# Kernel tuning notes

Measured on AMD Instinct MI355X. Metric: run time of the kernel, lower is better.

Reference implementation:

```python
import jax, jax.numpy as jnp
import numpy as np

B, S, D = 2, 2048, 1024
H_Q, H_KV, DK, DV = 16, 8, 64, 64
R = H_Q // H_KV  # q heads per kv head (GQA)
THETA = 10000.0


def setup_inputs() -> dict:
    key = jax.random.key(0)
    ks = jax.random.split(key, 12)
    inv_freq = 1.0 / (THETA ** (jnp.arange(0, DK, 2, dtype=jnp.float32) / DK))  # [DK/2]
    angles = jnp.arange(S, dtype=jnp.float32)[:, None] * inv_freq[None, :]      # [S, DK/2]
    scale = 0.02
    return {
        "x": jax.random.normal(ks[0], (B, S, D), jnp.float32),
        "Wq": jax.random.normal(ks[1], (D, H_Q * DK), jnp.float32) * scale,
        "bq": jnp.zeros((H_Q * DK,), jnp.float32),
        "Wk": jax.random.normal(ks[2], (D, H_KV * DK), jnp.float32) * scale,
        "bk": jnp.zeros((H_KV * DK,), jnp.float32),
        "Wv": jax.random.normal(ks[3], (D, H_KV * DV), jnp.float32) * scale,
        "bv": jnp.zeros((H_KV * DV,), jnp.float32),
        "Wo": jax.random.normal(ks[4], (H_Q * DV, D), jnp.float32) * scale,
        "bo": jnp.zeros((D,), jnp.float32),
        "freqs_cos": jnp.cos(angles),
        "freqs_sin": jnp.sin(angles),
        "attention_mask": jax.random.bernoulli(ks[5], 0.9, (B, S)),  # True = real token
    }


def _rope(t, cos, sin):
    # t: [B, S, H, Dh]; cos/sin: [S, Dh/2]. Complex rotation on interleaved pairs.
    tp = t.reshape(*t.shape[:-1], -1, 2)
    x1, x2 = tp[..., 0], tp[..., 1]
    c = cos[None, :, None, :]
    s = sin[None, :, None, :]
    o1 = x1 * c - x2 * s
    o2 = x1 * s + x2 * c
    return jnp.stack([o1, o2], axis=-1).reshape(t.shape)


def reference(x, Wq, bq, Wk, bk, Wv, bv, Wo, bo, freqs_cos, freqs_sin, attention_mask):
    b, s, _ = x.shape
    q = (x @ Wq + bq).reshape(b, s, H_Q, DK)
    k = (x @ Wk + bk).reshape(b, s, H_KV, DK)
    v = (x @ Wv + bv).reshape(b, s, H_KV, DV)
    q = _rope(q, freqs_cos, freqs_sin)
    k = _rope(k, freqs_cos, freqs_sin)
    q = q.transpose(0, 2, 1, 3)                      # [B, Hq, S, DK]
    k = jnp.repeat(k.transpose(0, 2, 1, 3), R, axis=1)  # GQA expand -> [B, Hq, S, DK]
    v = jnp.repeat(v.transpose(0, 2, 1, 3), R, axis=1)  # [B, Hq, S, DV]
    causal = jnp.tril(jnp.ones((s, s), dtype=bool))
    # Module does logical_or(padding, causal) -- replicated faithfully.
    mask = jnp.logical_or(attention_mask[:, None, None, :], causal[None, None])
    scale = 1.0 / jnp.sqrt(jnp.float32(DK))
    scores = jnp.einsum('bhqd,bhkd->bhqk', q, k) * scale
    scores = jnp.where(mask, scores, -jnp.inf)
    attn = jax.nn.softmax(scores, axis=-1)
    out = jnp.einsum('bhqk,bhkd->bhqd', attn, v)
    out = out.transpose(0, 2, 1, 3).reshape(b, s, H_Q * DV)
    return out @ Wo + bo
```

## Files before the change

kernel.cpp:

```cpp
#include <hip/hip_runtime.h>
#include <hip/hip_bf16.h>
#include <math.h>

typedef __attribute__((ext_vector_type(8))) short bf16x8;
typedef __attribute__((ext_vector_type(4))) float f32x4;

#define OFF_XB  0ull
#define OFF_WT  (8ull<<20)
#define OFF_WO  (12ull<<20)
#define OFF_QB  (14ull<<20)
#define OFF_KB  (22ull<<20)
#define OFF_VT  (26ull<<20)
#define OFF_AO  (30ull<<20)
#define OFF_MB  (38ull<<20)

#define QSCALE 0.18033688056680276f

__device__ inline unsigned pack_bf162(float a, float b) {
    __hip_bfloat162 t = __float22bfloat162_rn(make_float2(a, b));
    return *(unsigned*)&t;
}

__device__ inline float exp2_fast(float x) {
    float r;
    asm("v_exp_f32 %0, %1" : "=v"(r) : "v"(x));
    return r;
}

__device__ inline void gload16(const void* g, void* l) {
    __builtin_amdgcn_global_load_lds(
        (const __attribute__((address_space(1))) void*)g,
        (__attribute__((address_space(3))) void*)l, 16, 0, 0);
}

__launch_bounds__(256)
__global__ void prep_kernel(const float* __restrict__ x,
                            const float* __restrict__ Wq, const float* __restrict__ Wk,
                            const float* __restrict__ Wv, const float* __restrict__ Wo,
                            const void* __restrict__ mraw,
                            __hip_bfloat16* __restrict__ XB,
                            __hip_bfloat16* __restrict__ WT,
                            __hip_bfloat16* __restrict__ WoT,
                            float* __restrict__ mbias) {
    __shared__ float T[32][33];
    __shared__ int bad01, badf;
    const int tid = threadIdx.x;
    const int bid = blockIdx.x;
    if (bid < 1024) {
        const int base = bid * 4096;
#pragma unroll
        for (int i = 0; i < 4; ++i) {
            const int e = base + (i * 256 + tid) * 4;
            const float4 v = *(const float4*)&x[e];
            uint2 pk;
            pk.x = pack_bf162(v.x, v.y);
            pk.y = pack_bf162(v.z, v.w);
            *(uint2*)&XB[e] = pk;
        }
    } else if (bid < 4096) {
        const float* src; int ldn, nbase; __hip_bfloat16* dst; int n0, k0;
        if (bid < 3072) {
            const int tb = bid - 1024;
            const int kt = tb >> 6, nt = tb & 63;
            n0 = nt * 32; k0 = kt * 32; dst = WT;
            if (n0 < 1024)      { src = Wq; ldn = 1024; nbase = n0; }
            else if (n0 < 1536) { src = Wk; ldn = 512;  nbase = n0 - 1024; }
            else                { src = Wv; ldn = 512;  nbase = n0 - 1536; }
        } else {
            const int tb = bid - 3072;
            const int kt = tb >> 5, nt = tb & 31;
            n0 = nt * 32; k0 = kt * 32; dst = WoT;
            src = Wo; ldn = 1024; nbase = n0;
        }
        const int c = tid & 31, r0 = tid >> 5;
#pragma unroll
        for (int i = 0; i < 4; ++i)
            T[r0 + 8 * i][c] = src[(size_t)(k0 + r0 + 8 * i) * ldn + nbase + c];
        __syncthreads();
#pragma unroll
        for (int i = 0; i < 4; ++i) {
            const int nn = r0 + 8 * i;
            dst[(size_t)(n0 + nn) * 1024 + k0 + c] = __float2bfloat16(T[c][nn]);
        }
    } else {
        if (tid == 0) { bad01 = 0; badf = 0; }
        __syncthreads();
        const unsigned* w = (const unsigned*)mraw;
#pragma unroll
        for (int i = 0; i < 4; ++i) {
            const unsigned v = w[tid * 4 + i];
            if (v > 1u) atomicAdd(&bad01, 1);
            if (v != 0u && v != 0x3F800000u) atomicAdd(&badf, 1);
        }
        __syncthreads();
        const int fmt = (bad01 == 0) ? 0 : ((badf == 0) ? 1 : 2);
        for (int i = tid; i < 4096; i += 256) {
            bool on;
            if (fmt == 2) on = (((const unsigned char*)mraw)[i] != 0);
            else          on = (w[i] != 0u);
            mbias[i] = on ? 0.f : -1e30f;
        }
    }
}

#define QSTAGE(SEL, K0_) do {                                                    \
    _Pragma("unroll") for (int rnd_ = 0; rnd_ < 4; ++rnd_) {                     \
        const int off_ = rnd_ * 4096 + wid * 1024 + lane * 16;                   \
        const int row_ = off_ >> 7;                                              \
        const int ch_  = ((off_ >> 4) & 7) ^ (row_ & 7);                         \
        gload16((const char*)Ag + ((size_t)(n0 + row_) * 1024 + (K0_) + ch_ * 8) * 2, \
                Asm + (SEL) * 16384 + rnd_ * 4096 + wid * 1024);                 \
        gload16((const char*)Bg + ((size_t)(m0 + row_) * 1024 + (K0_) + ch_ * 8) * 2, \
                Bsm + (SEL) * 16384 + rnd_ * 4096 + wid * 1024);                 \
    }                                                                            \
} while (0)

__launch_bounds__(256)
__global__ void qkv_mfma_kernel(const __hip_bfloat16* __restrict__ XB,
                                const __hip_bfloat16* __restrict__ WT,
                                const float* __restrict__ bq, const float* __restrict__ bk,
                                const float* __restrict__ bv,
                                const float* __restrict__ fc, const float* __restrict__ fs,
                                __hip_bfloat16* __restrict__ QB,
                                __hip_bfloat16* __restrict__ KB,
                                __hip_bfloat16* __restrict__ VT) {
    __shared__ __attribute__((aligned(16))) char Asm[32768];
    __shared__ __attribute__((aligned(16))) char Bsm[32768];
    const int tid = threadIdx.x;
    const int lane = tid & 63, wid = tid >> 6;
    const int c = lane & 15, g = lane >> 4;
    const int n0 = blockIdx.x * 128, m0 = blockIdx.y * 128;
    const int wn = (wid >> 1) * 64, wm = (wid & 1) * 64;
    const __hip_bfloat16* Ag = WT;
    const __hip_bfloat16* Bg = XB;

    f32x4 acc[4][4];
#pragma unroll
    for (int ni = 0; ni < 4; ++ni)
#pragma unroll
        for (int mj = 0; mj < 4; ++mj) acc[ni][mj] = f32x4{0.f, 0.f, 0.f, 0.f};

    QSTAGE(0, 0);
    int cur = 0;
    for (int kt = 0; kt < 16; ++kt) {
        const int k0 = kt * 64;
        if (kt < 15) {
            QSTAGE(cur ^ 1, k0 + 64);
            asm volatile("s_waitcnt vmcnt(8)" ::: "memory");
        } else {
            asm volatile("s_waitcnt vmcnt(0)" ::: "memory");
        }
        __builtin_amdgcn_sched_barrier(0);
        __builtin_amdgcn_s_barrier();
        __builtin_amdgcn_sched_barrier(0);

        const char* Ac = Asm + cur * 16384;
        const char* Bc = Bsm + cur * 16384;
#pragma unroll
        for (int ks = 0; ks < 2; ++ks) {
            bf16x8 af[4], bfr[4];
#pragma unroll
            for (int t = 0; t < 4; ++t) {
                const int sl = ((g + 4 * ks) ^ (c & 7)) << 4;
                af[t]  = *(const bf16x8*)(Ac + (wn + 16 * t + c) * 128 + sl);
                bfr[t] = *(const bf16x8*)(Bc + (wm + 16 * t + c) * 128 + sl);
            }
#pragma unroll
            for (int ni = 0; ni < 4; ++ni)
#pragma unroll
                for (int mj = 0; mj < 4; ++mj)
                    acc[ni][mj] = __builtin_amdgcn_mfma_f32_16x16x32_bf16(
                        af[ni], bfr[mj], acc[ni][mj], 0, 0, 0);
        }
        __builtin_amdgcn_sched_barrier(0);
        __builtin_amdgcn_s_barrier();
        __builtin_amdgcn_sched_barrier(0);
        cur ^= 1;
    }

#pragma unroll
    for (int ni = 0; ni < 4; ++ni) {
        const int nb = n0 + wn + 16 * ni + 4 * g;
        const float* bias; int nloc;
        if (nb < 1024)      { bias = bq; nloc = nb; }
        else if (nb < 1536) { bias = bk; nloc = nb - 1024; }
        else                { bias = bv; nloc = nb - 1536; }
        const float4 b4 = *(const float4*)&bias[nloc];
        const int h = nloc >> 6, dk = nb & 63;
#pragma unroll
        for (int mj = 0; mj < 4; ++mj) {
            const int tok = m0 + wm + 16 * mj + c;
            const int bb = tok >> 11, sp = tok & 2047;
            float v0 = acc[ni][mj][0] + b4.x;
            float v1 = acc[ni][mj][1] + b4.y;
            float v2 = acc[ni][mj][2] + b4.z;
            float v3 = acc[ni][mj][3] + b4.w;
            if (nb < 1536) {
                const int p = sp * 32 + (dk >> 1);
                const float c0 = fc[p], s0 = fs[p];
                const float c1 = fc[p + 1], s1 = fs[p + 1];
                float o0 = v0 * c0 - v1 * s0, o1 = v0 * s0 + v1 * c0;
                float o2 = v2 * c1 - v3 * s1, o3 = v2 * s1 + v3 * c1;
                uint2 pk;
                if (nb < 1024) {
                    o0 *= QSCALE; o1 *= QSCALE; o2 *= QSCALE; o3 *= QSCALE;
                    pk.x = pack_bf162(o0, o1); pk.y = pack_bf162(o2, o3);
                    *(uint2*)&QB[(size_t)((bb * 16 + h) * 2048 + sp) * 64 + dk] = pk;
                } else {
                    pk.x = pack_bf162(o0, o1); pk.y = pack_bf162(o2, o3);
                    *(uint2*)&KB[(size_t)((bb * 8 + h) * 2048 + sp) * 64 + dk] = pk;
                }
            } else {
                const size_t vb = (size_t)((bb * 8 + h) * 64 + dk) * 2048 + sp;
                VT[vb]          = __float2bfloat16(v0);
                VT[vb + 2048]   = __float2bfloat16(v1);
                VT[vb + 4096]   = __float2bfloat16(v2);
                VT[vb + 6144]   = __float2bfloat16(v3);
            }
        }
    }
}

__launch_bounds__(256)
__global__ void out_mfma_kernel(const __hip_bfloat16* __restrict__ AOB,
                                const __hip_bfloat16* __restrict__ WoT,
                                const float* __restrict__ bo,
                                float* __restrict__ out) {
    __shared__ __attribute__((aligned(16))) char Asm[32768];
    __shared__ __attribute__((aligned(16))) char Bsm[32768];
    const int tid = threadIdx.x;
    const int lane = tid & 63, wid = tid >> 6;
    const int c = lane & 15, g = lane >> 4;
    const int n0 = blockIdx.x * 128, m0 = blockIdx.y * 128;
    const int wn = (wid >> 1) * 64, wm = (wid & 1) * 64;
    const __hip_bfloat16* Ag = WoT;
    const __hip_bfloat16* Bg = AOB;

    f32x4 acc[4][4];
#pragma unroll
    for (int ni = 0; ni < 4; ++ni)
#pragma unroll
        for (int mj = 0; mj < 4; ++mj) acc[ni][mj] = f32x4{0.f, 0.f, 0.f, 0.f};

    QSTAGE(0, 0);
    int cur = 0;
    for (int kt = 0; kt < 16; ++kt) {
        const int k0 = kt * 64;
        if (kt < 15) {
            QSTAGE(cur ^ 1, k0 + 64);
            asm volatile("s_waitcnt vmcnt(8)" ::: "memory");
        } else {
            asm volatile("s_waitcnt vmcnt(0)" ::: "memory");
        }
        __builtin_amdgcn_sched_barrier(0);
        __builtin_amdgcn_s_barrier();
        __builtin_amdgcn_sched_barrier(0);

        const char* Ac = Asm + cur * 16384;
        const char* Bc = Bsm + cur * 16384;
#pragma unroll
        for (int ks = 0; ks < 2; ++ks) {
            bf16x8 af[4], bfr[4];
#pragma unroll
            for (int t = 0; t < 4; ++t) {
                const int sl = ((g + 4 * ks) ^ (c & 7)) << 4;
                af[t]  = *(const bf16x8*)(Ac + (wn + 16 * t + c) * 128 + sl);
                bfr[t] = *(const bf16x8*)(Bc + (wm + 16 * t + c) * 128 + sl);
            }
#pragma unroll
            for (int ni = 0; ni < 4; ++ni)
#pragma unroll
                for (int mj = 0; mj < 4; ++mj)
                    acc[ni][mj] = __builtin_amdgcn_mfma_f32_16x16x32_bf16(
                        af[ni], bfr[mj], acc[ni][mj], 0, 0, 0);
        }
        __builtin_amdgcn_sched_barrier(0);
        __builtin_amdgcn_s_barrier();
        __builtin_amdgcn_sched_barrier(0);
        cur ^= 1;
    }
#pragma unroll
    for (int ni = 0; ni < 4; ++ni) {
        const int nb = n0 + wn + 16 * ni + 4 * g;
        const float4 b4 = *(const float4*)&bo[nb];
#pragma unroll
        for (int mj = 0; mj < 4; ++mj) {
            const int tok = m0 + wm + 16 * mj + c;
            const f32x4 a = acc[ni][mj];
            const float4 st = make_float4(a[0] + b4.x, a[1] + b4.y,
                                          a[2] + b4.z, a[3] + b4.w);
            *(float4*)&out[(size_t)tok * 1024 + nb] = st;
        }
    }
}


#define STAGE(BUFSEL, K0_) do {                                                  \
    _Pragma("unroll") for (int rnd_ = 0; rnd_ < 2; ++rnd_) {                     \
        const int off_ = rnd_ * 4096 + tid * 16;                                 \
        const int row_ = off_ >> 7;                                              \
        const int ch_  = ((off_ >> 4) & 7) ^ (row_ & 7);                         \
        gload16(Kh + (size_t)((K0_) + row_) * 64 + ch_ * 8,                      \
                Ksm + (BUFSEL) * 8192 + rnd_ * 4096 + wid * 1024);               \
        gload16(Vh + (size_t)row_ * 2048 + (K0_) + ch_ * 8,                      \
                Vsm + (BUFSEL) * 8192 + rnd_ * 4096 + wid * 1024);               \
    }                                                                            \
} while (0)

__launch_bounds__(256)
__global__ void attn_kernel(const __hip_bfloat16* __restrict__ QB,
                            const __hip_bfloat16* __restrict__ KB,
                            const __hip_bfloat16* __restrict__ VT,
                            const float* __restrict__ maskb,
                            __hip_bfloat16* __restrict__ AOB) {
    __shared__ __attribute__((aligned(16))) char Ksm[16384];
    __shared__ __attribute__((aligned(16))) char Vsm[16384];
    __shared__ char P_lds[4][4096];

    const int tid  = threadIdx.x;
    const int lane = tid & 63, wid = tid >> 6;
    const int c = lane & 15, g = lane >> 4;

    const int bid = blockIdx.x;
    const int o_  = (bid & 7) * 64 + (bid >> 3);
    const int qx = o_ & 15, h = (o_ >> 4) & 15, b = o_ >> 8;
    const int qb = qx * 128 + wid * 32;

    const __hip_bfloat16* Qh = QB + (size_t)(b * 16 + h)       * 2048 * 64;
    const __hip_bfloat16* Kh = KB + (size_t)(b * 8 + (h >> 1)) * 2048 * 64;
    const __hip_bfloat16* Vh = VT + (size_t)(b * 8 + (h >> 1)) * 64 * 2048;
    const float* mb = maskb + b * 2048;

    STAGE(0, 0);

    bf16x8 bq[2][2];
#pragma unroll
    for (int rt = 0; rt < 2; ++rt)
#pragma unroll
        for (int ks = 0; ks < 2; ++ks)
            bq[rt][ks] = *(const bf16x8*)&Qh[(size_t)(qb + 16 * rt + c) * 64
                                             + 32 * ks + 8 * g];
    __syncthreads();

    const short oneb = (short)0x3F80;
    const bf16x8 ones = {oneb, oneb, oneb, oneb, oneb, oneb, oneb, oneb};

    f32x4 o[2][4];
    f32x4 lacc[2];
#pragma unroll
    for (int rt = 0; rt < 2; ++rt) {
        lacc[rt] = f32x4{0.f, 0.f, 0.f, 0.f};
#pragma unroll
        for (int mt = 0; mt < 4; ++mt) o[rt][mt] = f32x4{0.f, 0.f, 0.f, 0.f};
    }
    float m_[2] = {-INFINITY, -INFINITY};

    char* Pw = &P_lds[wid][0];
    const int swz = (c & 7) << 4;

    int cur = 0;
    for (int kt = 0; kt < 32; ++kt) {
        const int k0 = kt * 64;
        if (kt < 31) {
            STAGE(cur ^ 1, k0 + 64);
            asm volatile("s_waitcnt vmcnt(4)" ::: "memory");
        } else {
            asm volatile("s_waitcnt vmcnt(0)" ::: "memory");
        }
        __builtin_amdgcn_sched_barrier(0);
        __builtin_amdgcn_s_barrier();
        __builtin_amdgcn_sched_barrier(0);

        const char* Kc = Ksm + cur * 8192;
        const char* Vc = Vsm + cur * 8192;

        bf16x8 ak[4][2];
#pragma unroll
        for (int mt = 0; mt < 4; ++mt)
#pragma unroll
            for (int ks = 0; ks < 2; ++ks)
                ak[mt][ks] = *(const bf16x8*)(Kc + (16 * mt + c) * 128
                                              + (((g + 4 * ks) ^ (c & 7)) << 4));

        const bool needb = (k0 + 63 > qb);
        f32x4 bv4[4];
        if (needb) {
#pragma unroll
            for (int mt = 0; mt < 4; ++mt)
                bv4[mt] = *(const f32x4*)&mb[k0 + 16 * mt + 4 * g];
        }

        __builtin_amdgcn_s_setprio(1);
        f32x4 st[2][4];
#pragma unroll
        for (int rt = 0; rt < 2; ++rt)
#pragma unroll
            for (int mt = 0; mt < 4; ++mt) {
                f32x4 z = f32x4{0.f, 0.f, 0.f, 0.f};
                z = __builtin_amdgcn_mfma_f32_16x16x32_bf16(ak[mt][0], bq[rt][0], z, 0, 0, 0);
                z = __builtin_amdgcn_mfma_f32_16x16x32_bf16(ak[mt][1], bq[rt][1], z, 0, 0, 0);
                st[rt][mt] = z;
            }
        __builtin_amdgcn_s_setprio(0);

        bf16x8 av[4][2];
#pragma unroll
        for (int mt = 0; mt < 4; ++mt)
#pragma unroll
            for (int ks = 0; ks < 2; ++ks)
                av[mt][ks] = *(const bf16x8*)(Vc + (16 * mt + c) * 128
                                              + (((g + 4 * ks) ^ (c & 7)) << 4));

#pragma unroll
        for (int rt = 0; rt < 2; ++rt) {
            const int qw = qb + 16 * rt;
            if (k0 + 63 <= qw) {
            } else if (k0 > qw + 15) {
#pragma unroll
                for (int mt = 0; mt < 4; ++mt)
                    st[rt][mt] = st[rt][mt] + bv4[mt];
            } else {
                const int qg = qw + c;
#pragma unroll
                for (int mt = 0; mt < 4; ++mt)
#pragma unroll
                    for (int r = 0; r < 4; ++r) {
                        const int kg = k0 + 16 * mt + 4 * g + r;
                        st[rt][mt][r] += (kg <= qg) ? 0.f : bv4[mt][r];
                    }
            }
            const f32x4 m01 = __builtin_elementwise_max(st[rt][0], st[rt][1]);
            const f32x4 m23 = __builtin_elementwise_max(st[rt][2], st[rt][3]);
            const f32x4 mv  = __builtin_elementwise_max(m01, m23);
            float pmax = fmaxf(fmaxf(mv[0], mv[1]), fmaxf(mv[2], mv[3]));
            pmax = fmaxf(pmax, __shfl_xor(pmax, 16));
            pmax = fmaxf(pmax, __shfl_xor(pmax, 32));
            if (!__all(pmax <= m_[rt] + 11.5f)) {
                const float mn = fmaxf(m_[rt], pmax);
                const float alpha = exp2_fast(m_[rt] - mn);
                m_[rt] = mn;
                lacc[rt][0] *= alpha;
#pragma unroll
                for (int mt = 0; mt < 4; ++mt) o[rt][mt] *= alpha;
            }
            const float mneg = m_[rt];
            const f32x4 m4 = {mneg, mneg, mneg, mneg};
#pragma unroll
            for (int mt = 0; mt < 4; ++mt) {
                const f32x4 e = st[rt][mt] - m4;
#pragma unroll
                for (int r = 0; r < 4; ++r)
                    st[rt][mt][r] = exp2_fast(e[r]);
            }

            char* Pr = Pw + rt * 2048 + c * 128;
#pragma unroll
            for (int mt = 0; mt < 4; ++mt) {
                const unsigned w0 = pack_bf162(st[rt][mt][0], st[rt][mt][1]);
                const unsigned w1 = pack_bf162(st[rt][mt][2], st[rt][mt][3]);
                *(unsigned long long*)(Pr + ((32 * mt + 8 * g) ^ swz)) =
                    (unsigned long long)w0 | ((unsigned long long)w1 << 32);
            }
        }

#pragma unroll
        for (int rt = 0; rt < 2; ++rt) {
            const char* Pr = Pw + rt * 2048 + c * 128;
            const bf16x8 pb0 = *(const bf16x8*)(Pr + ((16 * g) ^ swz));
            const bf16x8 pb1 = *(const bf16x8*)(Pr + ((64 + 16 * g) ^ swz));
            __builtin_amdgcn_s_setprio(1);
#pragma unroll
            for (int mt = 0; mt < 4; ++mt) {
                o[rt][mt] = __builtin_amdgcn_mfma_f32_16x16x32_bf16(av[mt][0], pb0, o[rt][mt], 0, 0, 0);
                o[rt][mt] = __builtin_amdgcn_mfma_f32_16x16x32_bf16(av[mt][1], pb1, o[rt][mt], 0, 0, 0);
            }
            lacc[rt] = __builtin_amdgcn_mfma_f32_16x16x32_bf16(ones, pb0, lacc[rt], 0, 0, 0);
            lacc[rt] = __builtin_amdgcn_mfma_f32_16x16x32_bf16(ones, pb1, lacc[rt], 0, 0, 0);
            __builtin_amdgcn_s_setprio(0);
        }

        __builtin_amdgcn_sched_barrier(0);
        __builtin_amdgcn_s_barrier();
        __builtin_amdgcn_sched_barrier(0);
        cur ^= 1;
    }

#pragma unroll
    for (int rt = 0; rt < 2; ++rt) {
        const float inv = 1.f / lacc[rt][0];
        const size_t tok = (size_t)(b * 2048 + qb + 16 * rt + c);
#pragma unroll
        for (int mt = 0; mt < 4; ++mt) {
            uint2 pk;
            pk.x = pack_bf162(o[rt][mt][0] * inv, o[rt][mt][1] * inv);
            pk.y = pack_bf162(o[rt][mt][2] * inv, o[rt][mt][3] * inv);
            *(uint2*)&AOB[tok * 1024 + h * 64 + 16 * mt + 4 * g] = pk;
        }
    }
}

extern "C" void kernel_launch(void* const* d_in, const int* in_sizes, int n_in,
                              void* d_out, int out_size, void* d_ws, size_t ws_size,
                              hipStream_t stream) {
    const float* x  = (const float*)d_in[0];
    const float* Wq = (const float*)d_in[1];
    const float* bq = (const float*)d_in[2];
    const float* Wk = (const float*)d_in[3];
    const float* bk = (const float*)d_in[4];
    const float* Wv = (const float*)d_in[5];
    const float* bv = (const float*)d_in[6];
    const float* Wo = (const float*)d_in[7];
    const float* bo = (const float*)d_in[8];
    const float* fc = (const float*)d_in[9];
    const float* fs = (const float*)d_in[10];
    const void*  am = d_in[11];

    char* ws = (char*)d_ws;
    __hip_bfloat16* XB  = (__hip_bfloat16*)(ws + OFF_XB);
    __hip_bfloat16* WT  = (__hip_bfloat16*)(ws + OFF_WT);
    __hip_bfloat16* WoT = (__hip_bfloat16*)(ws + OFF_WO);
    __hip_bfloat16* QB  = (__hip_bfloat16*)(ws + OFF_QB);
    __hip_bfloat16* KB  = (__hip_bfloat16*)(ws + OFF_KB);
    __hip_bfloat16* VT  = (__hip_bfloat16*)(ws + OFF_VT);
    __hip_bfloat16* AOB = (__hip_bfloat16*)(ws + OFF_AO);
    float* mbias = (float*)(ws + OFF_MB);
    float* out   = (float*)d_out;

    hipLaunchKernelGGL(prep_kernel, dim3(4097), dim3(256), 0, stream,
                       x, Wq, Wk, Wv, Wo, am, XB, WT, WoT, mbias);
    hipLaunchKernelGGL(qkv_mfma_kernel, dim3(16, 32), dim3(256), 0, stream,
                       XB, WT, bq, bk, bv, fc, fs, QB, KB, VT);
    hipLaunchKernelGGL(attn_kernel, dim3(512), dim3(256), 0, stream,
                       QB, KB, VT, mbias, AOB);
    hipLaunchKernelGGL(out_mfma_kernel, dim3(8, 32), dim3(256), 0, stream,
                       AOB, WoT, bo, out);
}
```

Before: 141.3 us.

## Widen attention KV tile to 128 keys with per-row-tile PV fusion

The attention loop now processes 128 keys per iteration instead of 64, halving the number of barriers and loop iterations. The double-buffered K/V tiles in LDS double to 32 KB each, and V uses a 16-way swizzle for its 256-byte rows. The P write and PV MFMAs are fused per row tile, V fragments are reloaded from LDS per k-slice, and launch bounds ask for 2 blocks per CU. This raises register pressure and LDS use (about 80 KB per block), which may limit occupancy.

After: 132.0 us (median of 2 runs). 6.6% less time.

```diff
diff --git a/kernel.cpp b/kernel.cpp
--- a/kernel.cpp
+++ b/kernel.cpp
@@ -295,26 +295,28 @@
 }
 
 
-#define STAGE(BUFSEL, K0_) do {                                                  \
-    _Pragma("unroll") for (int rnd_ = 0; rnd_ < 2; ++rnd_) {                     \
-        const int off_ = rnd_ * 4096 + tid * 16;                                 \
-        const int row_ = off_ >> 7;                                              \
-        const int ch_  = ((off_ >> 4) & 7) ^ (row_ & 7);                         \
-        gload16(Kh + (size_t)((K0_) + row_) * 64 + ch_ * 8,                      \
-                Ksm + (BUFSEL) * 8192 + rnd_ * 4096 + wid * 1024);               \
-        gload16(Vh + (size_t)row_ * 2048 + (K0_) + ch_ * 8,                      \
-                Vsm + (BUFSEL) * 8192 + rnd_ * 4096 + wid * 1024);               \
+#define STAGE128(SEL, K0_) do {                                                  \
+    _Pragma("unroll") for (int rnd_ = 0; rnd_ < 4; ++rnd_) {                     \
+        const int off_ = rnd_ * 4096 + wid * 1024 + lane * 16;                   \
+        const int kr_ = off_ >> 7;                                               \
+        const int kc_ = ((off_ >> 4) & 7) ^ (kr_ & 7);                           \
+        gload16(Kh + (size_t)((K0_) + kr_) * 64 + kc_ * 8,                       \
+                Ksm + (SEL) * 16384 + rnd_ * 4096 + wid * 1024);                 \
+        const int vr_ = off_ >> 8;                                               \
+        const int vc_ = ((off_ >> 4) & 15) ^ (vr_ & 15);                         \
+        gload16(Vh + (size_t)vr_ * 2048 + (K0_) + vc_ * 8,                       \
+                Vsm + (SEL) * 16384 + rnd_ * 4096 + wid * 1024);                 \
     }                                                                            \
 } while (0)
 
-__launch_bounds__(256)
+__launch_bounds__(256, 2)
 __global__ void attn_kernel(const __hip_bfloat16* __restrict__ QB,
                             const __hip_bfloat16* __restrict__ KB,
                             const __hip_bfloat16* __restrict__ VT,
                             const float* __restrict__ maskb,
                             __hip_bfloat16* __restrict__ AOB) {
-    __shared__ __attribute__((aligned(16))) char Ksm[16384];
-    __shared__ __attribute__((aligned(16))) char Vsm[16384];
+    __shared__ __attribute__((aligned(16))) char Ksm[32768];
+    __shared__ __attribute__((aligned(16))) char Vsm[32768];
     __shared__ char P_lds[4][4096];
 
     const int tid  = threadIdx.x;
@@ -331,7 +333,7 @@
     const __hip_bfloat16* Vh = VT + (size_t)(b * 8 + (h >> 1)) * 64 * 2048;
     const float* mb = maskb + b * 2048;
 
-    STAGE(0, 0);
+    STAGE128(0, 0);
 
     bf16x8 bq[2][2];
 #pragma unroll
@@ -355,15 +357,15 @@
     }
     float m_[2] = {-INFINITY, -INFINITY};
 
-    char* Pw = &P_lds[wid][0];
+    char* Pr = &P_lds[wid][0] + c * 256;
     const int swz = (c & 7) << 4;
 
     int cur = 0;
-    for (int kt = 0; kt < 32; ++kt) {
-        const int k0 = kt * 64;
-        if (kt < 31) {
-            STAGE(cur ^ 1, k0 + 64);
-            asm volatile("s_waitcnt vmcnt(4)" ::: "memory");
+    for (int kt = 0; kt < 16; ++kt) {
+        const int k0 = kt * 128;
+        if (kt < 15) {
+            STAGE128(cur ^ 1, k0 + 128);
+            asm volatile("s_waitcnt vmcnt(8)" ::: "memory");
         } else {
             asm volatile("s_waitcnt vmcnt(0)" ::: "memory");
         }
@@ -371,67 +373,65 @@
         __builtin_amdgcn_s_barrier();
         __builtin_amdgcn_sched_barrier(0);
 
-        const char* Kc = Ksm + cur * 8192;
-        const char* Vc = Vsm + cur * 8192;
-
-        bf16x8 ak[4][2];
-#pragma unroll
-        for (int mt = 0; mt < 4; ++mt)
-#pragma unroll
-            for (int ks = 0; ks < 2; ++ks)
-                ak[mt][ks] = *(const bf16x8*)(Kc + (16 * mt + c) * 128
-                                              + (((g + 4 * ks) ^ (c & 7)) << 4));
-
-        const bool needb = (k0 + 63 > qb);
-        f32x4 bv4[4];
+        const char* Kc = Ksm + cur * 16384;
+        const char* Vc = Vsm + cur * 16384;
+
+        const bool needb = (k0 + 127 > qb);
+        f32x4 bv4[8];
         if (needb) {
 #pragma unroll
+            for (int mt = 0; mt < 8; ++mt)
+                bv4[mt] = *(const f32x4*)&mb[k0 + 16 * mt + 4 * g];
+        }
+
+        f32x4 st[2][8];
+        __builtin_amdgcn_s_setprio(1);
+#pragma unroll
+        for (int hf = 0; hf < 2; ++hf) {
+            bf16x8 ak[4][2];
+#pragma unroll
             for (int mt = 0; mt < 4; ++mt)
-                bv4[mt] = *(const f32x4*)&mb[k0 + 16 * mt + 4 * g];
-        }
-
-        __builtin_amdgcn_s_setprio(1);
-        f32x4 st[2][4];
-#pragma unroll
-        for (int rt = 0; rt < 2; ++rt)
-#pragma unroll
-            for (int mt = 0; mt < 4; ++mt) {
-                f32x4 z = f32x4{0.f, 0.f, 0.f, 0.f};
-                z = __builtin_amdgcn_mfma_f32_16x16x32_bf16(ak[mt][0], bq[rt][0], z, 0, 0, 0);
-                z = __builtin_amdgcn_mfma_f32_16x16x32_bf16(ak[mt][1], bq[rt][1], z, 0, 0, 0);
-                st[rt][mt] = z;
-            }
+#pragma unroll
+                for (int ks = 0; ks < 2; ++ks)
+                    ak[mt][ks] = *(const bf16x8*)(Kc + (64 * hf + 16 * mt + c) * 128
+                                                  + (((g + 4 * ks) ^ (c & 7)) << 4));
+#pragma unroll
+            for (int rt = 0; rt < 2; ++rt)
+#pragma unroll
+                for (int mt = 0; mt < 4; ++mt) {
+                    f32x4 z = f32x4{0.f, 0.f, 0.f, 0.f};
+                    z = __builtin_amdgcn_mfma_f32_16x16x32_bf16(ak[mt][0], bq[rt][0], z, 0, 0, 0);
+                    z = __builtin_amdgcn_mfma_f32_16x16x32_bf16(ak[mt][1], bq[rt][1], z, 0, 0, 0);
+                    st[rt][4 * hf + mt] = z;
+                }
+        }
         __builtin_amdgcn_s_setprio(0);
-
-        bf16x8 av[4][2];
-#pragma unroll
-        for (int mt = 0; mt < 4; ++mt)
-#pragma unroll
-            for (int ks = 0; ks < 2; ++ks)
-                av[mt][ks] = *(const bf16x8*)(Vc + (16 * mt + c) * 128
-                                              + (((g + 4 * ks) ^ (c & 7)) << 4));
 
 #pragma unroll
         for (int rt = 0; rt < 2; ++rt) {
             const int qw = qb + 16 * rt;
-            if (k0 + 63 <= qw) {
+            if (k0 + 127 <= qw) {
             } else if (k0 > qw + 15) {
 #pragma unroll
-                for (int mt = 0; mt < 4; ++mt)
+                for (int mt = 0; mt < 8; ++mt)
                     st[rt][mt] = st[rt][mt] + bv4[mt];
             } else {
                 const int qg = qw + c;
 #pragma unroll
-                for (int mt = 0; mt < 4; ++mt)
+                for (int mt = 0; mt < 8; ++mt)
 #pragma unroll
                     for (int r = 0; r < 4; ++r) {
                         const int kg = k0 + 16 * mt + 4 * g + r;
                         st[rt][mt][r] += (kg <= qg) ? 0.f : bv4[mt][r];
                     }
             }
-            const f32x4 m01 = __builtin_elementwise_max(st[rt][0], st[rt][1]);
-            const f32x4 m23 = __builtin_elementwise_max(st[rt][2], st[rt][3]);
-            const f32x4 mv  = __builtin_elementwise_max(m01, m23);
+            const f32x4 a0 = __builtin_elementwise_max(st[rt][0], st[rt][1]);
+            const f32x4 a1 = __builtin_elementwise_max(st[rt][2], st[rt][3]);
+            const f32x4 a2 = __builtin_elementwise_max(st[rt][4], st[rt][5]);
+            const f32x4 a3 = __builtin_elementwise_max(st[rt][6], st[rt][7]);
+            const f32x4 b0 = __builtin_elementwise_max(a0, a1);
+            const f32x4 b1 = __builtin_elementwise_max(a2, a3);
+            const f32x4 mv = __builtin_elementwise_max(b0, b1);
             float pmax = fmaxf(fmaxf(mv[0], mv[1]), fmaxf(mv[2], mv[3]));
             pmax = fmaxf(pmax, __shfl_xor(pmax, 16));
             pmax = fmaxf(pmax, __shfl_xor(pmax, 32));
@@ -446,36 +446,35 @@
             const float mneg = m_[rt];
             const f32x4 m4 = {mneg, mneg, mneg, mneg};
 #pragma unroll
-            for (int mt = 0; mt < 4; ++mt) {
+            for (int mt = 0; mt < 8; ++mt) {
                 const f32x4 e = st[rt][mt] - m4;
 #pragma unroll
                 for (int r = 0; r < 4; ++r)
                     st[rt][mt][r] = exp2_fast(e[r]);
             }
 
-            char* Pr = Pw + rt * 2048 + c * 128;
-#pragma unroll
-            for (int mt = 0; mt < 4; ++mt) {
+#pragma unroll
+            for (int mt = 0; mt < 8; ++mt) {
                 const unsigned w0 = pack_bf162(st[rt][mt][0], st[rt][mt][1]);
                 const unsigned w1 = pack_bf162(st[rt][mt][2], st[rt][mt][3]);
                 *(unsigned long long*)(Pr + ((32 * mt + 8 * g) ^ swz)) =
                     (unsigned long long)w0 | ((unsigned long long)w1 << 32);
             }
-        }
-
-#pragma unroll
-        for (int rt = 0; rt < 2; ++rt) {
-            const char* Pr = Pw + rt * 2048 + c * 128;
-            const bf16x8 pb0 = *(const bf16x8*)(Pr + ((16 * g) ^ swz));
-            const bf16x8 pb1 = *(const bf16x8*)(Pr + ((64 + 16 * g) ^ swz));
+
             __builtin_amdgcn_s_setprio(1);
 #pragma unroll
-            for (int mt = 0; mt < 4; ++mt) {
-                o[rt][mt] = __builtin_amdgcn_mfma_f32_16x16x32_bf16(av[mt][0], pb0, o[rt][mt], 0, 0, 0);
-                o[rt][mt] = __builtin_amdgcn_mfma_f32_16x16x32_bf16(av[mt][1], pb1, o[rt][mt], 0, 0, 0);
-            }
-            lacc[rt] = __builtin_amdgcn_mfma_f32_16x16x32_bf16(ones, pb0, lacc[rt], 0, 0, 0);
-            lacc[rt] = __builtin_amdgcn_mfma_f32_16x16x32_bf16(ones, pb1, lacc[rt], 0, 0, 0);
+            for (int ks = 0; ks < 4; ++ks) {
+                const bf16x8 pb = *(const bf16x8*)(Pr + ((64 * ks + 16 * g) ^ swz));
+                bf16x8 av[4];
+#pragma unroll
+                for (int mt = 0; mt < 4; ++mt)
+                    av[mt] = *(const bf16x8*)(Vc + (16 * mt + c) * 256
+                                              + (((4 * ks + g) ^ (c & 15)) << 4));
+#pragma unroll
+                for (int mt = 0; mt < 4; ++mt)
+                    o[rt][mt] = __builtin_amdgcn_mfma_f32_16x16x32_bf16(av[mt], pb, o[rt][mt], 0, 0, 0);
+                lacc[rt] = __builtin_amdgcn_mfma_f32_16x16x32_bf16(ones, pb, lacc[rt], 0, 0, 0);
+            }
             __builtin_amdgcn_s_setprio(0);
         }
 
```
